# Kernel tuning notes

Measured on AMD Instinct MI355X. Metric: run time of the kernel, lower is better.

Reference implementation:

```python
import jax, jax.numpy as jnp
import numpy as np

N_GRAPHS = 64
NEG_SLOPE = 0.2


def gat_conv(x, src, dst, n_nodes, W, a_src, a_dst, b):
    # PyG GATConv (heads=1): h = x @ W; e_ij = LeakyReLU(a_src.h_j + a_dst.h_i)
    # softmax over incoming edges of each destination node, then weighted sum.
    h = x @ W                                  # [N, F_out]
    alpha_s = h @ a_src                        # [N]
    alpha_d = h @ a_dst                        # [N]
    e = jax.nn.leaky_relu(alpha_s[src] + alpha_d[dst], NEG_SLOPE)  # [E]
    m = jax.ops.segment_max(e, dst, num_segments=n_nodes)          # stable softmax
    ex = jnp.exp(e - m[dst])
    denom = jax.ops.segment_sum(ex, dst, num_segments=n_nodes)
    alpha = ex / (denom[dst] + 1e-16)                              # [E]
    out = jax.ops.segment_sum(h[src] * alpha[:, None], dst, num_segments=n_nodes)
    return out + b


def setup_inputs() -> dict:
    key = jax.random.key(0)
    ks = jax.random.split(key, 16)
    N, E, D, H = 50000, 1600000, 128, 64
    x = jax.random.normal(ks[0], (N, D), dtype=jnp.float32)
    edge_index = jax.random.randint(ks[1], (2, E), 0, N, dtype=jnp.int64)
    batch = jnp.sort(jax.random.randint(ks[2], (N,), 0, N_GRAPHS, dtype=jnp.int64))
    def glorot(k, shape):
        lim = float(np.sqrt(6.0 / (shape[0] + shape[-1])))
        return jax.random.uniform(k, shape, jnp.float32, -lim, lim)
    return {
        "x": x, "edge_index": edge_index, "batch": batch,
        "W1": glorot(ks[3], (D, H)),
        "a_src1": glorot(ks[4], (H,)), "a_dst1": glorot(ks[5], (H,)),
        "b1": jnp.zeros((H,), jnp.float32),
        "W2": glorot(ks[6], (H, 2 * H)),
        "a_src2": glorot(ks[7], (2 * H,)), "a_dst2": glorot(ks[8], (2 * H,)),
        "b2": jnp.zeros((2 * H,), jnp.float32),
        "Wfc": glorot(ks[9], (2 * H, H)),
        "bfc": jnp.zeros((H,), jnp.float32),
    }


def reference(x, edge_index, batch, W1, a_src1, a_dst1, b1, W2, a_src2, a_dst2, b2, Wfc, bfc):
    n = x.shape[0]
    # PyG GATConv default add_self_loops=True
    loops = jnp.arange(n, dtype=edge_index.dtype)
    src = jnp.concatenate([edge_index[0], loops])
    dst = jnp.concatenate([edge_index[1], loops])
    h = jax.nn.relu(gat_conv(x, src, dst, n, W1, a_src1, a_dst1, b1))
    h = jax.nn.relu(gat_conv(h, src, dst, n, W2, a_src2, a_dst2, b2))
    # global_mean_pool over batch vector
    sums = jax.ops.segment_sum(h, batch, num_segments=N_GRAPHS)
    cnts = jax.ops.segment_sum(jnp.ones((n,), h.dtype), batch, num_segments=N_GRAPHS)
    pooled = sums / jnp.maximum(cnts, 1.0)[:, None]
    # dropout is identity in eval mode
    return pooled @ Wfc + bfc
```

## Files before the change

### kernel.cpp

```cpp
#include <hip/hip_runtime.h>
#include <hip/hip_fp16.h>

#define WAVE 64

constexpr int D_IN = 128;
constexpr int F1 = 64;
constexpr int F2 = 128;
constexpr int NG = 64;
constexpr float NEG = 0.2f;
constexpr int NBLK1 = 512;

using f16x8 = __attribute__((ext_vector_type(8))) _Float16;
using f32x4 = __attribute__((ext_vector_type(4))) float;

__device__ __forceinline__ float lrelu(float x){ return x > 0.f ? x : NEG * x; }

__global__ void k_hist(const int* __restrict__ src, const int* __restrict__ dst,
                       int E, int N, int NB, int chunk, int* __restrict__ cnt1){
  __shared__ int hist[256];
  int b = blockIdx.x;
  for (int t = threadIdx.x; t < NB; t += blockDim.x) hist[t] = 0;
  __syncthreads();
  int Et = E + N;
  int s0 = b * chunk, s1 = min(s0 + chunk, Et);
  for (int i = s0 + (int)threadIdx.x; i < s1; i += (int)blockDim.x){
    int d = (i < E) ? dst[i] : (i - E);
    atomicAdd(&hist[d >> 8], 1);
  }
  __syncthreads();
  for (int t = threadIdx.x; t < NB; t += blockDim.x) cnt1[t * NBLK1 + b] = hist[t];
}

__global__ void k_colscan(int* __restrict__ cnt1, int* __restrict__ btot){
  __shared__ int lds[256];
  int b = blockIdx.x;
  int t = threadIdx.x;
  int v0 = cnt1[b * NBLK1 + 2 * t], v1 = cnt1[b * NBLK1 + 2 * t + 1];
  int p = v0 + v1;
  lds[t] = p; __syncthreads();
  #pragma unroll
  for (int s = 1; s < 256; s <<= 1){
    int u = (t >= s) ? lds[t - s] : 0;
    __syncthreads(); lds[t] += u; __syncthreads();
  }
  int epre = lds[t] - p;
  cnt1[b * NBLK1 + 2 * t] = epre;
  cnt1[b * NBLK1 + 2 * t + 1] = epre + v0;
  if (t == 255) btot[b] = lds[255];
}

__global__ void k_bucketscan(const int* __restrict__ btot, int NB, int Et,
                             int* __restrict__ bbase, int* __restrict__ off, int N){
  __shared__ int lds[256];
  int t = threadIdx.x;
  int v = (t < NB) ? btot[t] : 0;
  lds[t] = v; __syncthreads();
  #pragma unroll
  for (int s = 1; s < 256; s <<= 1){
    int u = (t >= s) ? lds[t - s] : 0;
    __syncthreads(); lds[t] += u; __syncthreads();
  }
  if (t < NB) bbase[t] = lds[t] - v;
  if (t == 0){ bbase[NB] = Et; off[N] = Et; }
}

__global__ void k_scatter1(const int* __restrict__ src, const int* __restrict__ dst,
                           int E, int N, int NB, int chunk,
                           const int* __restrict__ cnt1, const int* __restrict__ bbase,
                           int* __restrict__ tmp){
  __shared__ int cur[256];
  int b = blockIdx.x;
  for (int t = threadIdx.x; t < NB; t += blockDim.x) cur[t] = bbase[t] + cnt1[t * NBLK1 + b];
  __syncthreads();
  int Et = E + N;
  int s0 = b * chunk, s1 = min(s0 + chunk, Et);
  for (int i = s0 + (int)threadIdx.x; i < s1; i += (int)blockDim.x){
    int s, d;
    if (i < E){ s = src[i]; d = dst[i]; } else { s = d = i - E; }
    int bk = d >> 8;
    int p = atomicAdd(&cur[bk], 1);
    tmp[p] = (s << 8) | (d & 255);
  }
}

__global__ void k_sort2(const int* __restrict__ tmp, const int* __restrict__ bbase,
                        int N, int* __restrict__ off, int* __restrict__ csr_src){
  __shared__ int hist[256];
  __shared__ int pre[256];
  int b = blockIdx.x;
  int t = threadIdx.x;
  hist[t] = 0;
  __syncthreads();
  int g0 = bbase[b], g1 = bbase[b + 1];
  for (int i = g0 + t; i < g1; i += 256) atomicAdd(&hist[tmp[i] & 255], 1);
  __syncthreads();
  int v = hist[t];
  pre[t] = v; __syncthreads();
  #pragma unroll
  for (int s = 1; s < 256; s <<= 1){
    int u = (t >= s) ? pre[t - s] : 0;
    __syncthreads(); pre[t] += u; __syncthreads();
  }
  int ex = pre[t] - v;
  int node = (b << 8) + t;
  if (node < N) off[node] = g0 + ex;
  hist[t] = ex;
  __syncthreads();
  for (int i = g0 + t; i < g1; i += 256){
    int e = tmp[i];
    int p = g0 + atomicAdd(&hist[e & 255], 1);
    csr_src[p] = e >> 8;
  }
}

template<int FI, int FO, bool AF32>
__global__ void k_gemm_mfma(const void* __restrict__ Av, const float* __restrict__ W,
                            const float* __restrict__ avs, const float* __restrict__ avd,
                            __half* __restrict__ Ch, float* __restrict__ as_, float* __restrict__ ad_,
                            int M){
  constexpr int NT = FO / 16;
  constexpr int KT = FI / 32;
  constexpr int MT = 2;
  __shared__ _Float16 blds[NT * KT * 64 * 8];

  int tid = threadIdx.x;
  for (int fl = tid; fl < NT * KT * 64; fl += 256){
    int l = fl & 63, kt = (fl >> 6) % KT, nt = fl / (64 * KT);
    int n = nt * 16 + (l & 15), kb = kt * 32 + (l >> 4) * 8;
    f16x8 v;
    #pragma unroll
    for (int i = 0; i < 8; ++i) v[i] = (_Float16)W[(size_t)(kb + i) * FO + n];
    *(f16x8*)&blds[(size_t)fl * 8] = v;
  }
  __syncthreads();

  int lane = tid & 63, wave = tid >> 6;
  int rbase = lane & 15, kgrp = lane >> 4;
  int r0 = blockIdx.x * (MT * 16 * 4) + wave * (MT * 16);

  f32x4 c[MT][NT];
  #pragma unroll
  for (int mt = 0; mt < MT; ++mt)
    #pragma unroll
    for (int nt = 0; nt < NT; ++nt)
      c[mt][nt] = (f32x4){0.f, 0.f, 0.f, 0.f};

  for (int kt = 0; kt < KT; ++kt){
    f16x8 a[MT];
    #pragma unroll
    for (int mt = 0; mt < MT; ++mt){
      int arow = min(r0 + mt * 16 + rbase, M - 1);
      if (AF32){
        const float* ap = (const float*)Av + (size_t)arow * FI + kt * 32 + kgrp * 8;
        float4 p0 = *(const float4*)ap;
        float4 p1 = *(const float4*)(ap + 4);
        a[mt][0] = (_Float16)p0.x; a[mt][1] = (_Float16)p0.y;
        a[mt][2] = (_Float16)p0.z; a[mt][3] = (_Float16)p0.w;
        a[mt][4] = (_Float16)p1.x; a[mt][5] = (_Float16)p1.y;
        a[mt][6] = (_Float16)p1.z; a[mt][7] = (_Float16)p1.w;
      } else {
        const __half* ap = (const __half*)Av + (size_t)arow * FI + kt * 32 + kgrp * 8;
        a[mt] = *(const f16x8*)ap;
      }
    }
    #pragma unroll
    for (int nt = 0; nt < NT; ++nt){
      f16x8 b = *(f16x8*)&blds[(size_t)((nt * KT + kt) * 64 + lane) * 8];
      #pragma unroll
      for (int mt = 0; mt < MT; ++mt)
        c[mt][nt] = __builtin_amdgcn_mfma_f32_16x16x32_f16(a[mt], b, c[mt][nt], 0, 0, 0);
    }
  }

  float avs_v[NT], avd_v[NT];
  #pragma unroll
  for (int nt = 0; nt < NT; ++nt){
    avs_v[nt] = avs[nt * 16 + rbase];
    avd_v[nt] = avd[nt * 16 + rbase];
  }
  #pragma unroll
  for (int mt = 0; mt < MT; ++mt){
    #pragma unroll
    for (int i = 0; i < 4; ++i){
      int grow = r0 + mt * 16 + kgrp * 4 + i;
      bool ok = grow < M;
      float s1 = 0.f, s2 = 0.f;
      #pragma unroll
      for (int nt = 0; nt < NT; ++nt){
        float d = c[mt][nt][i];
        if (ok) Ch[(size_t)grow * FO + nt * 16 + rbase] = __float2half(d);
        s1 += d * avs_v[nt];
        s2 += d * avd_v[nt];
      }
      #pragma unroll
      for (int msk = 1; msk <= 8; msk <<= 1){
        s1 += __shfl_xor(s1, msk);
        s2 += __shfl_xor(s2, msk);
      }
      if (ok && rbase == 0){ as_[grow] = s1; ad_[grow] = s2; }
    }
  }
}

template<int F, bool OUT16>
__global__ void k_node(const int* __restrict__ off, const int* __restrict__ csr_src,
                       const __half* __restrict__ h, const float* __restrict__ as_,
                       const float* __restrict__ ad_, const float* __restrict__ bias,
                       __half* __restrict__ outh, float* __restrict__ outf, int N){
  constexpr int CPL = F / WAVE;
  int lane = threadIdx.x & (WAVE - 1);
  int node = (blockIdx.x * blockDim.x + threadIdx.x) >> 6;
  if (node >= N) return;
  int o0 = off[node], o1 = off[node + 1];
  float add = ad_[node];
  float acc[CPL];
  #pragma unroll
  for (int c = 0; c < CPL; ++c) acc[c] = 0.f;
  float wsum = 0.f;
  int j = o0;
  for (; j + 8 <= o1; j += 8){
    int ss[8];
    #pragma unroll
    for (int u = 0; u < 8; ++u) ss[u] = csr_src[j + u];
    float w[8];
    #pragma unroll
    for (int u = 0; u < 8; ++u) w[u] = __expf(lrelu(as_[ss[u]] + add));
    if (CPL == 1){
      float r[8];
      #pragma unroll
      for (int u = 0; u < 8; ++u) r[u] = __half2float(h[(size_t)ss[u] * F + lane]);
      #pragma unroll
      for (int u = 0; u < 8; ++u){ wsum += w[u]; acc[0] += w[u] * r[u]; }
    } else {
      float2 r[8];
      #pragma unroll
      for (int u = 0; u < 8; ++u){
        __half2 hv = *(const __half2*)(h + (size_t)ss[u] * F + 2 * lane);
        r[u] = __half22float2(hv);
      }
      #pragma unroll
      for (int u = 0; u < 8; ++u){
        wsum += w[u];
        acc[0] += w[u] * r[u].x;
        acc[1] += w[u] * r[u].y;
      }
    }
  }
  for (; j < o1; ++j){
    int s = csr_src[j];
    float w = __expf(lrelu(as_[s] + add));
    wsum += w;
    if (CPL == 1){
      acc[0] += w * __half2float(h[(size_t)s * F + lane]);
    } else {
      __half2 hv = *(const __half2*)(h + (size_t)s * F + 2 * lane);
      float2 r = __half22float2(hv);
      acc[0] += w * r.x;
      acc[1] += w * r.y;
    }
  }
  float inv = 1.f / (wsum + 1e-16f);
  #pragma unroll
  for (int c = 0; c < CPL; ++c){
    int col = (CPL == 1) ? lane : (2 * lane + c);
    float v = fmaxf(acc[c] * inv + bias[col], 0.f);
    if (OUT16) outh[(size_t)node * F + col] = __float2half(v);
    else       outf[(size_t)node * F + col] = v;
  }
}

__global__ void k_pool(const float* __restrict__ h, const int* __restrict__ batch,
                       float* __restrict__ pool, int* __restrict__ cnt, int N, int strip){
  int f = threadIdx.x;
  int n0 = blockIdx.x * strip;
  if (n0 >= N) return;
  int n1 = min(n0 + strip, N);
  int g = batch[n0];
  float acc = 0.f;
  int c = 0;
  for (int n = n0; n < n1; ++n){
    int gn = batch[n];
    if (gn != g){
      atomicAdd(&pool[g * F2 + f], acc);
      if (f == 0) atomicAdd(&cnt[g], c);
      acc = 0.f; c = 0; g = gn;
    }
    acc += h[(size_t)n * F2 + f];
    c++;
  }
  atomicAdd(&pool[g * F2 + f], acc);
  if (f == 0) atomicAdd(&cnt[g], c);
}

__global__ void k_fc(const float* __restrict__ pool, const int* __restrict__ cnt,
                     const float* __restrict__ Wfc, const float* __restrict__ bfc,
                     float* __restrict__ out){
  int g = blockIdx.x, o = threadIdx.x;
  __shared__ float p[F2];
  float invc = 1.f / fmaxf((float)cnt[g], 1.f);
  for (int k = threadIdx.x; k < F2; k += 64) p[k] = pool[g * F2 + k] * invc;
  __syncthreads();
  float acc = bfc[o];
  for (int k = 0; k < F2; ++k) acc += p[k] * Wfc[k * 64 + o];
  out[g * 64 + o] = acc;
}

extern "C" void kernel_launch(void* const* d_in, const int* in_sizes, int n_in,
                              void* d_out, int out_size, void* d_ws, size_t ws_size,
                              hipStream_t stream){
  const float* x    = (const float*)d_in[0];
  const int*   edge = (const int*)d_in[1];
  const int*   batch= (const int*)d_in[2];
  const float* W1   = (const float*)d_in[3];
  const float* av_s1= (const float*)d_in[4];
  const float* av_d1= (const float*)d_in[5];
  const float* b1   = (const float*)d_in[6];
  const float* W2   = (const float*)d_in[7];
  const float* av_s2= (const float*)d_in[8];
  const float* av_d2= (const float*)d_in[9];
  const float* b2   = (const float*)d_in[10];
  const float* Wfc  = (const float*)d_in[11];
  const float* bfc  = (const float*)d_in[12];
  float* out = (float*)d_out;

  const int N  = in_sizes[2];
  const int E  = in_sizes[1] / 2;
  const int Et = E + N;
  const int NB = (N + 255) >> 8;
  const int* src = edge;
  const int* dst = edge + E;

  char* p = (char*)d_ws;
  auto alloc = [&](size_t bytes)->void*{
    void* r = (void*)p;
    p += (bytes + 255) & ~(size_t)255;
    return r;
  };
  __half* h1  = (__half*)alloc((size_t)N * F1 * 2);
  __half* h1r = (__half*)alloc((size_t)N * F1 * 2);
  __half* h2  = (__half*)alloc((size_t)N * F2 * 2);
  float* h2r  = (float*)alloc((size_t)N * F2 * 4);
  float* as1  = (float*)alloc((size_t)N * 4);
  float* ad1  = (float*)alloc((size_t)N * 4);
  float* as2  = (float*)alloc((size_t)N * 4);
  float* ad2  = (float*)alloc((size_t)N * 4);
  float* pool = (float*)alloc((size_t)NG * F2 * 4);
  int* off    = (int*)alloc((size_t)(N + 1) * 4);
  int* csr_src= (int*)alloc((size_t)Et * 4);
  int* tmp    = (int*)alloc((size_t)Et * 4);
  int* cnt1   = (int*)alloc((size_t)256 * NBLK1 * 4);
  int* btot   = (int*)alloc((size_t)256 * 4);
  int* bbase  = (int*)alloc((size_t)257 * 4);
  int* cnt    = (int*)alloc((size_t)NG * 4);

  hipMemsetAsync(pool, 0, (size_t)NG * F2 * 4, stream);
  hipMemsetAsync(cnt, 0, (size_t)NG * 4, stream);

  int chunk = (Et + NBLK1 - 1) / NBLK1;
  k_hist<<<NBLK1, 256, 0, stream>>>(src, dst, E, N, NB, chunk, cnt1);
  k_colscan<<<NB, 256, 0, stream>>>(cnt1, btot);
  k_bucketscan<<<1, 256, 0, stream>>>(btot, NB, Et, bbase, off, N);
  k_scatter1<<<NBLK1, 256, 0, stream>>>(src, dst, E, N, NB, chunk, cnt1, bbase, tmp);
  k_sort2<<<NB, 256, 0, stream>>>(tmp, bbase, N, off, csr_src);

  int gemm_blocks = (N + 127) / 128;
  int node_blocks = (N + 3) / 4;

  k_gemm_mfma<D_IN, F1, true><<<gemm_blocks, 256, 0, stream>>>(x, W1, av_s1, av_d1,
                                                               h1, as1, ad1, N);
  k_node<F1, true><<<node_blocks, 256, 0, stream>>>(off, csr_src, h1, as1, ad1, b1,
                                                    h1r, nullptr, N);

  k_gemm_mfma<F1, F2, false><<<gemm_blocks, 256, 0, stream>>>(h1r, W2, av_s2, av_d2,
                                                              h2, as2, ad2, N);
  k_node<F2, false><<<node_blocks, 256, 0, stream>>>(off, csr_src, h2, as2, ad2, b2,
                                                     nullptr, h2r, N);

  int strip = 128;
  int pool_blocks = (N + strip - 1) / strip;
  k_pool<<<pool_blocks, F2, 0, stream>>>(h2r, batch, pool, cnt, N, strip);
  k_fc<<<NG, 64, 0, stream>>>(pool, cnt, Wfc, bfc, out);
}
```

Baseline: 234.0 us.

## Precompute edge attention weights in separate kernel and store layer-2 output as fp16

```diff
diff --git a/kernel.cpp b/kernel.cpp
--- a/kernel.cpp
+++ b/kernel.cpp
@@ -84,7 +84,8 @@
 }
 
 __global__ void k_sort2(const int* __restrict__ tmp, const int* __restrict__ bbase,
-                        int N, int* __restrict__ off, int* __restrict__ csr_src){
+                        int N, int* __restrict__ off, int* __restrict__ csr_src,
+                        int* __restrict__ dst_arr){
   __shared__ int hist[256];
   __shared__ int pre[256];
   int b = blockIdx.x;
@@ -110,7 +111,17 @@
     int e = tmp[i];
     int p = g0 + atomicAdd(&hist[e & 255], 1);
     csr_src[p] = e >> 8;
-  }
+    dst_arr[p] = (b << 8) | (e & 255);
+  }
+}
+
+__global__ void k_weight(const int* __restrict__ csr_src, const int* __restrict__ dst_arr,
+                         const float* __restrict__ as_, const float* __restrict__ ad_,
+                         float* __restrict__ we, int Et){
+  int i = blockIdx.x * blockDim.x + threadIdx.x;
+  int stride = gridDim.x * blockDim.x;
+  for (; i < Et; i += stride)
+    we[i] = __expf(lrelu(as_[csr_src[i]] + ad_[dst_arr[i]]));
 }
 
 template<int FI, int FO, bool AF32>
@@ -202,74 +213,60 @@
   }
 }
 
-template<int F, bool OUT16>
+template<int F>
 __global__ void k_node(const int* __restrict__ off, const int* __restrict__ csr_src,
-                       const __half* __restrict__ h, const float* __restrict__ as_,
-                       const float* __restrict__ ad_, const float* __restrict__ bias,
-                       __half* __restrict__ outh, float* __restrict__ outf, int N){
+                       const float* __restrict__ we, const __half* __restrict__ h,
+                       const float* __restrict__ bias, __half* __restrict__ outh, int N){
   constexpr int CPL = F / WAVE;
   int lane = threadIdx.x & (WAVE - 1);
-  int node = (blockIdx.x * blockDim.x + threadIdx.x) >> 6;
+  int wid = (int)((blockIdx.x * blockDim.x + threadIdx.x) >> 6);
+  int node = __builtin_amdgcn_readfirstlane(wid);
   if (node >= N) return;
   int o0 = off[node], o1 = off[node + 1];
-  float add = ad_[node];
-  float acc[CPL];
-  #pragma unroll
-  for (int c = 0; c < CPL; ++c) acc[c] = 0.f;
-  float wsum = 0.f;
+  const __half* hb = h + ((CPL == 1) ? lane : 2 * lane);
+  float acc0 = 0.f, acc1 = 0.f, wsum = 0.f;
   int j = o0;
   for (; j + 8 <= o1; j += 8){
-    int ss[8];
-    #pragma unroll
-    for (int u = 0; u < 8; ++u) ss[u] = csr_src[j + u];
-    float w[8];
-    #pragma unroll
-    for (int u = 0; u < 8; ++u) w[u] = __expf(lrelu(as_[ss[u]] + add));
-    if (CPL == 1){
-      float r[8];
-      #pragma unroll
-      for (int u = 0; u < 8; ++u) r[u] = __half2float(h[(size_t)ss[u] * F + lane]);
-      #pragma unroll
-      for (int u = 0; u < 8; ++u){ wsum += w[u]; acc[0] += w[u] * r[u]; }
-    } else {
-      float2 r[8];
-      #pragma unroll
-      for (int u = 0; u < 8; ++u){
-        __half2 hv = *(const __half2*)(h + (size_t)ss[u] * F + 2 * lane);
-        r[u] = __half22float2(hv);
+    int s[8]; float w[8];
+    #pragma unroll
+    for (int u = 0; u < 8; ++u){ s[u] = csr_src[j + u]; w[u] = we[j + u]; }
+    #pragma unroll
+    for (int u = 0; u < 8; ++u){
+      if (CPL == 1){
+        float r = __half2float(hb[(size_t)s[u] * F]);
+        acc0 += w[u] * r;
+      } else {
+        float2 r = __half22float2(*(const __half2*)(hb + (size_t)s[u] * F));
+        acc0 += w[u] * r.x;
+        acc1 += w[u] * r.y;
       }
-      #pragma unroll
-      for (int u = 0; u < 8; ++u){
-        wsum += w[u];
-        acc[0] += w[u] * r[u].x;
-        acc[1] += w[u] * r[u].y;
-      }
+      wsum += w[u];
     }
   }
   for (; j < o1; ++j){
     int s = csr_src[j];
-    float w = __expf(lrelu(as_[s] + add));
+    float w = we[j];
+    if (CPL == 1){
+      acc0 += w * __half2float(hb[(size_t)s * F]);
+    } else {
+      float2 r = __half22float2(*(const __half2*)(hb + (size_t)s * F));
+      acc0 += w * r.x;
+      acc1 += w * r.y;
+    }
     wsum += w;
-    if (CPL == 1){
-      acc[0] += w * __half2float(h[(size_t)s * F + lane]);
-    } else {
-      __half2 hv = *(const __half2*)(h + (size_t)s * F + 2 * lane);
-      float2 r = __half22float2(hv);
-      acc[0] += w * r.x;
-      acc[1] += w * r.y;
-    }
   }
   float inv = 1.f / (wsum + 1e-16f);
-  #pragma unroll
-  for (int c = 0; c < CPL; ++c){
-    int col = (CPL == 1) ? lane : (2 * lane + c);
-    float v = fmaxf(acc[c] * inv + bias[col], 0.f);
-    if (OUT16) outh[(size_t)node * F + col] = __float2half(v);
-    else       outf[(size_t)node * F + col] = v;
-  }
-}
-
-__global__ void k_pool(const float* __restrict__ h, const int* __restrict__ batch,
+  if (CPL == 1){
+    float v = fmaxf(acc0 * inv + bias[lane], 0.f);
+    outh[(size_t)node * F + lane] = __float2half(v);
+  } else {
+    float v0 = fmaxf(acc0 * inv + bias[2 * lane], 0.f);
+    float v1 = fmaxf(acc1 * inv + bias[2 * lane + 1], 0.f);
+    *(__half2*)(outh + (size_t)node * F + 2 * lane) = __floats2half2_rn(v0, v1);
+  }
+}
+
+__global__ void k_pool(const __half* __restrict__ h, const int* __restrict__ batch,
                        float* __restrict__ pool, int* __restrict__ cnt, int N, int strip){
   int f = threadIdx.x;
   int n0 = blockIdx.x * strip;
@@ -285,7 +282,7 @@
       if (f == 0) atomicAdd(&cnt[g], c);
       acc = 0.f; c = 0; g = gn;
     }
-    acc += h[(size_t)n * F2 + f];
+    acc += __half2float(h[(size_t)n * F2 + f]);
     c++;
   }
   atomicAdd(&pool[g * F2 + f], acc);
@@ -339,14 +336,16 @@
   __half* h1  = (__half*)alloc((size_t)N * F1 * 2);
   __half* h1r = (__half*)alloc((size_t)N * F1 * 2);
   __half* h2  = (__half*)alloc((size_t)N * F2 * 2);
-  float* h2r  = (float*)alloc((size_t)N * F2 * 4);
+  __half* h2r = (__half*)alloc((size_t)N * F2 * 2);
   float* as1  = (float*)alloc((size_t)N * 4);
   float* ad1  = (float*)alloc((size_t)N * 4);
   float* as2  = (float*)alloc((size_t)N * 4);
   float* ad2  = (float*)alloc((size_t)N * 4);
   float* pool = (float*)alloc((size_t)NG * F2 * 4);
+  float* we   = (float*)alloc((size_t)Et * 4);
   int* off    = (int*)alloc((size_t)(N + 1) * 4);
   int* csr_src= (int*)alloc((size_t)Et * 4);
+  int* dst_arr= (int*)alloc((size_t)Et * 4);
   int* tmp    = (int*)alloc((size_t)Et * 4);
   int* cnt1   = (int*)alloc((size_t)256 * NBLK1 * 4);
   int* btot   = (int*)alloc((size_t)256 * 4);
@@ -361,20 +360,21 @@
   k_colscan<<<NB, 256, 0, stream>>>(cnt1, btot);
   k_bucketscan<<<1, 256, 0, stream>>>(btot, NB, Et, bbase, off, N);
   k_scatter1<<<NBLK1, 256, 0, stream>>>(src, dst, E, N, NB, chunk, cnt1, bbase, tmp);
-  k_sort2<<<NB, 256, 0, stream>>>(tmp, bbase, N, off, csr_src);
+  k_sort2<<<NB, 256, 0, stream>>>(tmp, bbase, N, off, csr_src, dst_arr);
 
   int gemm_blocks = (N + 127) / 128;
   int node_blocks = (N + 3) / 4;
+  int wblocks = 2048;
 
   k_gemm_mfma<D_IN, F1, true><<<gemm_blocks, 256, 0, stream>>>(x, W1, av_s1, av_d1,
                                                                h1, as1, ad1, N);
-  k_node<F1, true><<<node_blocks, 256, 0, stream>>>(off, csr_src, h1, as1, ad1, b1,
-                                                    h1r, nullptr, N);
+  k_weight<<<wblocks, 256, 0, stream>>>(csr_src, dst_arr, as1, ad1, we, Et);
+  k_node<F1><<<node_blocks, 256, 0, stream>>>(off, csr_src, we, h1, b1, h1r, N);
 
   k_gemm_mfma<F1, F2, false><<<gemm_blocks, 256, 0, stream>>>(h1r, W2, av_s2, av_d2,
                                                               h2, as2, ad2, N);
-  k_node<F2, false><<<node_blocks, 256, 0, stream>>>(off, csr_src, h2, as2, ad2, b2,
-                                                     nullptr, h2r, N);
+  k_weight<<<wblocks, 256, 0, stream>>>(csr_src, dst_arr, as2, ad2, we, Et);
+  k_node<F2><<<node_blocks, 256, 0, stream>>>(off, csr_src, we, h2, b2, h2r, N);
 
   int strip = 128;
   int pool_blocks = (N + strip - 1) / strip;
```

After: 235.0 us. No clear change (+0.4%).
